# Optimization experiments

Hardware: AMD Instinct MI355X
Metric: run time of the kernel (lower is better)

## Reference

```python
import jax, jax.numpy as jnp
import numpy as np
import math

K_DIM = 1024
HEADS = 16

def setup_inputs() -> dict:
    key = jax.random.key(0)
    ks = jax.random.split(key, 6)
    b, N, k = 4, 2048, K_DIM
    sc = 1.0 / math.sqrt(k)
    return {
        "x": jax.random.normal(ks[0], (b, N, k), dtype=jnp.float32),
        "Wk": jax.random.normal(ks[1], (k, k), dtype=jnp.float32) * sc,
        "Wq": jax.random.normal(ks[2], (k, k), dtype=jnp.float32) * sc,
        "Wv": jax.random.normal(ks[3], (k, k), dtype=jnp.float32) * sc,
        "Wu": jax.random.normal(ks[4], (k, k), dtype=jnp.float32) * sc,
        "bu": jax.random.normal(ks[5], (k,), dtype=jnp.float32) * 0.01,
    }

def reference(x, Wk, Wq, Wv, Wu, bu):
    b, N, k = x.shape
    h = HEADS
    s = k // h
    # torch Linear: y = x @ W^T
    Q = (x @ Wq.T).reshape(b, N, h, s).transpose(0, 2, 1, 3)  # [b,h,N,s]
    Kh = (x @ Wk.T).reshape(b, N, h, s).transpose(0, 2, 1, 3)
    V = (x @ Wv.T).reshape(b, N, h, s).transpose(0, 2, 1, 3)
    scores = jnp.einsum('bhid,bhjd->bhij', Q, Kh) / math.sqrt(s)  # [b,h,N,N]
    attn = jax.nn.softmax(scores, axis=-1)
    out = jnp.einsum('bhij,bhjd->bhid', attn, V)  # [b,h,N,s]
    out = out.transpose(0, 2, 1, 3).reshape(b, N, k)
    return out @ Wu.T + bu
```

## Files before the change

kernel.cpp:

```cpp
#include <hip/hip_runtime.h>

typedef __bf16 bf16;
typedef __bf16 bf16x4 __attribute__((ext_vector_type(4)));
typedef __bf16 bf16x8 __attribute__((ext_vector_type(8)));
typedef float  f32x4  __attribute__((ext_vector_type(4)));

#define MFMA16(a, b, c) __builtin_amdgcn_mfma_f32_16x16x32_bf16((a), (b), (c), 0, 0, 0)

__device__ __forceinline__ void async_copy16(const void* g, void* l) {
  __builtin_amdgcn_global_load_lds(
      (const __attribute__((address_space(1))) unsigned int*)g,
      (__attribute__((address_space(3))) unsigned int*)l, 16, 0, 0);
}

struct CvtArgs {
  const float* src[5];
  bf16* dst[5];
  int blk_start[6];
};
__global__ void k_cvt_all(CvtArgs a) {
  int b = blockIdx.x;
  int seg = 0;
#pragma unroll
  for (int s = 1; s < 5; ++s) seg += (b >= a.blk_start[s]);
  int i = (b - a.blk_start[seg]) * 2048 + threadIdx.x * 8;
  float4 v0 = *(const float4*)(a.src[seg] + i);
  float4 v1 = *(const float4*)(a.src[seg] + i + 4);
  float sc = (seg == 1) ? 0.18033688f : 1.0f;
  bf16x8 o = { (bf16)(v0.x * sc), (bf16)(v0.y * sc), (bf16)(v0.z * sc), (bf16)(v0.w * sc),
               (bf16)(v1.x * sc), (bf16)(v1.y * sc), (bf16)(v1.z * sc), (bf16)(v1.w * sc) };
  *(bf16x8*)(a.dst[seg] + i) = o;
}

template <int OUTF32, int PERMB = 0>
__device__ __forceinline__ void gemm128_body(
    const bf16* __restrict__ A, const bf16* __restrict__ B, void* __restrict__ Cp,
    const float* __restrict__ bias, int m0, int n0, int N, int K) {
  __shared__ alignas(16) bf16 As[2][128 * 32];
  __shared__ alignas(16) bf16 Bs[2][128 * 32];
  const int tid = threadIdx.x;
  const int lane = tid & 63;
  const int w = tid >> 6;
  const int quad = lane >> 4;
  const int l16 = lane & 15;
  const int wr = (w >> 1) * 64;
  const int wc = (w & 1) * 64;

  const int srow = tid >> 2;
  const int skk = (tid & 3) * 8;
  const int srowB =
      PERMB ? ((srow & 0x23) | ((srow & 0x04) << 2) | ((srow & 0x18) >> 1)) : srow;
  const bf16* Ag = A + (long)(m0 + srow) * K + skk;
  const bf16* Bg = B + (long)(n0 + srowB) * K + skk;
  const long half = 64L * K;
  bf16* AsW0 = As[0] + w * 512;
  bf16* BsW0 = Bs[0] + w * 512;
  bf16* AsW1 = As[1] + w * 512;
  bf16* BsW1 = Bs[1] + w * 512;

  f32x4 acc[4][4];
#pragma unroll
  for (int i = 0; i < 4; ++i)
#pragma unroll
    for (int j = 0; j < 4; ++j) acc[i][j] = (f32x4){0.f, 0.f, 0.f, 0.f};

  for (int k0 = 0; k0 < K; k0 += 64) {
    async_copy16(Ag + k0, AsW0);
    async_copy16(Ag + half + k0, AsW0 + 2048);
    async_copy16(Bg + k0, BsW0);
    async_copy16(Bg + half + k0, BsW0 + 2048);
    async_copy16(Ag + k0 + 32, AsW1);
    async_copy16(Ag + half + k0 + 32, AsW1 + 2048);
    async_copy16(Bg + k0 + 32, BsW1);
    async_copy16(Bg + half + k0 + 32, BsW1 + 2048);
    __syncthreads();
#pragma unroll
    for (int p = 0; p < 2; ++p) {
      const bf16* AsP = As[p];
      const bf16* BsP = Bs[p];
      bf16x8 af[4], bfr[4];
#pragma unroll
      for (int i = 0; i < 4; ++i)
        af[i] = *(const bf16x8*)&AsP[(wr + i * 16 + l16) * 32 + quad * 8];
#pragma unroll
      for (int j = 0; j < 4; ++j)
        bfr[j] = *(const bf16x8*)&BsP[(wc + j * 16 + l16) * 32 + quad * 8];
#pragma unroll
      for (int i = 0; i < 4; ++i)
#pragma unroll
        for (int j = 0; j < 4; ++j) acc[i][j] = MFMA16(af[i], bfr[j], acc[i][j]);
    }
    __syncthreads();
  }

#pragma unroll
  for (int i = 0; i < 4; ++i)
#pragma unroll
    for (int j = 0; j < 4; ++j)
#pragma unroll
      for (int r = 0; r < 4; ++r) {
        long row = m0 + wr + i * 16 + quad * 4 + r;
        int col = n0 + wc + j * 16 + l16;
        if (OUTF32)
          ((float*)Cp)[row * N + col] = acc[i][j][r] + bias[col];
        else
          ((bf16*)Cp)[row * N + col] = (bf16)acc[i][j][r];
      }
}

__global__ __launch_bounds__(256, 4) void k_gemm_qkv(
    const bf16* __restrict__ xb, const bf16* __restrict__ Wqk, bf16* __restrict__ QKb,
    const bf16* __restrict__ Wvb, bf16* __restrict__ VtG) {
  int bid = blockIdx.x;
  if (bid < 1024) {
    gemm128_body<0, 0>(xb, Wqk, QKb, nullptr,
                       (bid & 63) * 128, (bid >> 6) * 128, 2048, 1024);
  } else {
    int id = bid - 1024;
    gemm128_body<0, 1>(Wvb, xb, VtG, nullptr,
                       (id >> 6) * 128, (id & 63) * 128, 8192, 1024);
  }
}

__global__ __launch_bounds__(256, 4) void k_gemm_out(
    const bf16* __restrict__ Ab, const bf16* __restrict__ Wub, float* __restrict__ out,
    const float* __restrict__ bu) {
  gemm128_body<1, 0>(Ab, Wub, out, bu, blockIdx.x * 128, blockIdx.y * 128, 1024, 1024);
}

__global__ __launch_bounds__(256, 2) void k_attn(
    const bf16* __restrict__ Q, const bf16* __restrict__ Kb,
    const bf16* __restrict__ Vt, bf16* __restrict__ O) {
  __shared__ alignas(16) bf16 Ks[2][64 * 64];
  __shared__ alignas(16) bf16 Vs[2][64 * 64];

  const int tid = threadIdx.x;
  const int lane = tid & 63;
  const int w = tid >> 6;
  const int quad = lane >> 4;
  const int l16 = lane & 15;
  const int hsw = l16 & 7;
  const int bh = blockIdx.x;
  const int qt = blockIdx.y;
  const int bb = bh >> 4;
  const int h = bh & 15;
  const int hoff = h * 64;
  const long rowQ0 = (long)bb * 2048 + qt * 256;
  const long kv0 = (long)bb * 2048;

  bf16x8 bq[4][2];
#pragma unroll
  for (int g = 0; g < 4; ++g)
#pragma unroll
    for (int ss = 0; ss < 2; ++ss)
      bq[g][ss] = *(const bf16x8*)(Q + (rowQ0 + w * 64 + g * 16 + l16) * 2048 +
                                   hoff + ss * 32 + quad * 8);

  f32x4 accO[4][4];
  f32x4 accS[4];
#pragma unroll
  for (int g = 0; g < 4; ++g) {
    accS[g] = (f32x4){0.f, 0.f, 0.f, 0.f};
#pragma unroll
    for (int t = 0; t < 4; ++t) accO[g][t] = (f32x4){0.f, 0.f, 0.f, 0.f};
  }

  const int rr = tid >> 3;
  const int cc8 = ((tid & 7) ^ (rr & 7)) * 8;
  const bf16* ksrc = Kb + (kv0 + rr) * 2048 + hoff + cc8;
  const bf16* vsrc = Vt + (long)(hoff + rr) * 8192 + kv0 + cc8;
  const int dstOff = w * 512;

  async_copy16(ksrc, Ks[0] + dstOff);
  async_copy16(ksrc + 32 * 2048, Ks[0] + 2048 + dstOff);
  async_copy16(vsrc, Vs[0] + dstOff);
  async_copy16(vsrc + 32 * 8192, Vs[0] + 2048 + dstOff);
  ksrc += 64 * 2048;
  vsrc += 64;

  const bf16 onev = (bf16)1.0f;
  const bf16x8 ones8 = {onev, onev, onev, onev, onev, onev, onev, onev};

  for (int kt = 0; kt < 32; ++kt) {
    __syncthreads();
    if (kt < 31) {
      bf16* kb = Ks[(kt + 1) & 1];
      bf16* vb = Vs[(kt + 1) & 1];
      async_copy16(ksrc, kb + dstOff);
      async_copy16(ksrc + 32 * 2048, kb + 2048 + dstOff);
      async_copy16(vsrc, vb + dstOff);
      async_copy16(vsrc + 32 * 8192, vb + 2048 + dstOff);
      ksrc += 64 * 2048;
      vsrc += 64;
    }
    const bf16* kbuf = Ks[kt & 1];
    const bf16* vbuf = Vs[kt & 1];

    bf16x8 ak[4][2];
#pragma unroll
    for (int mt = 0; mt < 4; ++mt) {
      const int rb = (mt * 16 + l16) * 64;
      ak[mt][0] = *(const bf16x8*)&kbuf[rb + ((quad ^ hsw) * 8)];
      ak[mt][1] = *(const bf16x8*)&kbuf[rb + (((4 + quad) ^ hsw) * 8)];
    }
    bf16x8 bv[2][4];
#pragma unroll
    for (int ss = 0; ss < 2; ++ss)
#pragma unroll
      for (int t = 0; t < 4; ++t) {
        const int rb = (t * 16 + l16) * 64;
        bv[ss][t] = *(const bf16x8*)&vbuf[rb + (((ss * 4 + quad) ^ hsw) * 8)];
      }

#pragma unroll
    for (int g = 0; g < 4; ++g) {
      f32x4 st[4];
      __builtin_amdgcn_s_setprio(1);
#pragma unroll
      for (int mt = 0; mt < 4; ++mt) {
        st[mt] = (f32x4){0.f, 0.f, 0.f, 0.f};
        st[mt] = MFMA16(ak[mt][0], bq[g][0], st[mt]);
        st[mt] = MFMA16(ak[mt][1], bq[g][1], st[mt]);
      }
      __builtin_amdgcn_s_setprio(0);
      bf16x8 apf[2];
#pragma unroll
      for (int mt = 0; mt < 4; ++mt) {
#pragma unroll
        for (int r = 0; r < 4; ++r) {
          float pv = __builtin_amdgcn_exp2f(st[mt][r]);
          apf[mt >> 1][(mt & 1) * 4 + r] = (bf16)pv;
        }
      }
      __builtin_amdgcn_s_setprio(1);
#pragma unroll
      for (int ss = 0; ss < 2; ++ss) {
#pragma unroll
        for (int t = 0; t < 4; ++t)
          accO[g][t] = MFMA16(apf[ss], bv[ss][t], accO[g][t]);
        accS[g] = MFMA16(apf[ss], ones8, accS[g]);
      }
      __builtin_amdgcn_s_setprio(0);
    }
  }

#pragma unroll
  for (int g = 0; g < 4; ++g)
#pragma unroll
    for (int r = 0; r < 4; ++r) {
      float inv = 1.f / accS[g][r];
      long row = rowQ0 + w * 64 + g * 16 + quad * 4 + r;
#pragma unroll
      for (int t = 0; t < 4; ++t)
        O[row * 1024 + hoff + t * 16 + l16] = (bf16)(accO[g][t][r] * inv);
    }
}

extern "C" void kernel_launch(void* const* d_in, const int* in_sizes, int n_in,
                              void* d_out, int out_size, void* d_ws, size_t ws_size,
                              hipStream_t stream) {
  const float* x  = (const float*)d_in[0];
  const float* Wk = (const float*)d_in[1];
  const float* Wq = (const float*)d_in[2];
  const float* Wv = (const float*)d_in[3];
  const float* Wu = (const float*)d_in[4];
  const float* bu = (const float*)d_in[5];
  float* out = (float*)d_out;

  const int XE = 4 * 2048 * 1024;
  const int WE = 1024 * 1024;

  bf16* p = (bf16*)d_ws;
  bf16* xb   = p; p += XE;
  bf16* Wqkb = p; p += 2 * WE;
  bf16* Wvb  = p; p += WE;
  bf16* Wub  = p; p += WE;
  bf16* QKb  = p; p += 2 * XE;
  bf16* VtG  = p; p += XE;
  bf16* Ab   = p; p += XE;

  CvtArgs ca;
  ca.src[0] = x;  ca.dst[0] = xb;
  ca.src[1] = Wq; ca.dst[1] = Wqkb;
  ca.src[2] = Wk; ca.dst[2] = Wqkb + WE;
  ca.src[3] = Wv; ca.dst[3] = Wvb;
  ca.src[4] = Wu; ca.dst[4] = Wub;
  ca.blk_start[0] = 0;
  ca.blk_start[1] = XE / 2048;
  ca.blk_start[2] = ca.blk_start[1] + WE / 2048;
  ca.blk_start[3] = ca.blk_start[2] + WE / 2048;
  ca.blk_start[4] = ca.blk_start[3] + WE / 2048;
  ca.blk_start[5] = ca.blk_start[4] + WE / 2048;
  k_cvt_all<<<ca.blk_start[5], 256, 0, stream>>>(ca);

  k_gemm_qkv<<<1536, 256, 0, stream>>>(xb, Wqkb, QKb, Wvb, VtG);

  k_attn<<<dim3(64, 8), 256, 0, stream>>>(QKb, QKb + 1024, VtG, Ab);

  k_gemm_out<<<dim3(64, 8), 256, 0, stream>>>(Ab, Wub, out, bu);
}
```

Measured before the change: 243.7 us.

## Fuse attention and output projection into one cooperative kernel with grid sync

```diff
diff --git a/kernel.cpp b/kernel.cpp
--- a/kernel.cpp
+++ b/kernel.cpp
@@ -1,4 +1,7 @@
 #include <hip/hip_runtime.h>
+#include <hip/hip_cooperative_groups.h>
+
+namespace cg = cooperative_groups;
 
 typedef __bf16 bf16;
 typedef __bf16 bf16x4 __attribute__((ext_vector_type(4)));
@@ -35,9 +38,8 @@
 template <int OUTF32, int PERMB = 0>
 __device__ __forceinline__ void gemm128_body(
     const bf16* __restrict__ A, const bf16* __restrict__ B, void* __restrict__ Cp,
-    const float* __restrict__ bias, int m0, int n0, int N, int K) {
-  __shared__ alignas(16) bf16 As[2][128 * 32];
-  __shared__ alignas(16) bf16 Bs[2][128 * 32];
+    const float* __restrict__ bias, int m0, int n0, int N, int K,
+    bf16* AsS, bf16* BsS) {
   const int tid = threadIdx.x;
   const int lane = tid & 63;
   const int w = tid >> 6;
@@ -53,10 +55,10 @@
   const bf16* Ag = A + (long)(m0 + srow) * K + skk;
   const bf16* Bg = B + (long)(n0 + srowB) * K + skk;
   const long half = 64L * K;
-  bf16* AsW0 = As[0] + w * 512;
-  bf16* BsW0 = Bs[0] + w * 512;
-  bf16* AsW1 = As[1] + w * 512;
-  bf16* BsW1 = Bs[1] + w * 512;
+  bf16* AsW0 = AsS + w * 512;
+  bf16* BsW0 = BsS + w * 512;
+  bf16* AsW1 = AsS + 4096 + w * 512;
+  bf16* BsW1 = BsS + 4096 + w * 512;
 
   f32x4 acc[4][4];
 #pragma unroll
@@ -76,8 +78,8 @@
     __syncthreads();
 #pragma unroll
     for (int p = 0; p < 2; ++p) {
-      const bf16* AsP = As[p];
-      const bf16* BsP = Bs[p];
+      const bf16* AsP = AsS + p * 4096;
+      const bf16* BsP = BsS + p * 4096;
       bf16x8 af[4], bfr[4];
 #pragma unroll
       for (int i = 0; i < 4; ++i)
@@ -111,29 +113,32 @@
 __global__ __launch_bounds__(256, 4) void k_gemm_qkv(
     const bf16* __restrict__ xb, const bf16* __restrict__ Wqk, bf16* __restrict__ QKb,
     const bf16* __restrict__ Wvb, bf16* __restrict__ VtG) {
+  __shared__ alignas(16) bf16 As[2 * 128 * 32];
+  __shared__ alignas(16) bf16 Bs[2 * 128 * 32];
   int bid = blockIdx.x;
   if (bid < 1024) {
     gemm128_body<0, 0>(xb, Wqk, QKb, nullptr,
-                       (bid & 63) * 128, (bid >> 6) * 128, 2048, 1024);
+                       (bid & 63) * 128, (bid >> 6) * 128, 2048, 1024, As, Bs);
   } else {
     int id = bid - 1024;
     gemm128_body<0, 1>(Wvb, xb, VtG, nullptr,
-                       (id >> 6) * 128, (id & 63) * 128, 8192, 1024);
+                       (id >> 6) * 128, (id & 63) * 128, 8192, 1024, As, Bs);
   }
 }
 
 __global__ __launch_bounds__(256, 4) void k_gemm_out(
     const bf16* __restrict__ Ab, const bf16* __restrict__ Wub, float* __restrict__ out,
     const float* __restrict__ bu) {
-  gemm128_body<1, 0>(Ab, Wub, out, bu, blockIdx.x * 128, blockIdx.y * 128, 1024, 1024);
-}
-
-__global__ __launch_bounds__(256, 2) void k_attn(
+  __shared__ alignas(16) bf16 As[2 * 128 * 32];
+  __shared__ alignas(16) bf16 Bs[2 * 128 * 32];
+  gemm128_body<1, 0>(Ab, Wub, out, bu, blockIdx.x * 128, blockIdx.y * 128, 1024, 1024,
+                     As, Bs);
+}
+
+__device__ __forceinline__ void attn_body(
     const bf16* __restrict__ Q, const bf16* __restrict__ Kb,
-    const bf16* __restrict__ Vt, bf16* __restrict__ O) {
-  __shared__ alignas(16) bf16 Ks[2][64 * 64];
-  __shared__ alignas(16) bf16 Vs[2][64 * 64];
-
+    const bf16* __restrict__ Vt, bf16* __restrict__ Ab,
+    bf16* KsB, bf16* VsB) {
   const int tid = threadIdx.x;
   const int lane = tid & 63;
   const int w = tid >> 6;
@@ -171,10 +176,10 @@
   const bf16* vsrc = Vt + (long)(hoff + rr) * 8192 + kv0 + cc8;
   const int dstOff = w * 512;
 
-  async_copy16(ksrc, Ks[0] + dstOff);
-  async_copy16(ksrc + 32 * 2048, Ks[0] + 2048 + dstOff);
-  async_copy16(vsrc, Vs[0] + dstOff);
-  async_copy16(vsrc + 32 * 8192, Vs[0] + 2048 + dstOff);
+  async_copy16(ksrc, KsB + dstOff);
+  async_copy16(ksrc + 32 * 2048, KsB + 2048 + dstOff);
+  async_copy16(vsrc, VsB + dstOff);
+  async_copy16(vsrc + 32 * 8192, VsB + 2048 + dstOff);
   ksrc += 64 * 2048;
   vsrc += 64;
 
@@ -184,8 +189,8 @@
   for (int kt = 0; kt < 32; ++kt) {
     __syncthreads();
     if (kt < 31) {
-      bf16* kb = Ks[(kt + 1) & 1];
-      bf16* vb = Vs[(kt + 1) & 1];
+      bf16* kb = KsB + ((kt + 1) & 1) * 4096;
+      bf16* vb = VsB + ((kt + 1) & 1) * 4096;
       async_copy16(ksrc, kb + dstOff);
       async_copy16(ksrc + 32 * 2048, kb + 2048 + dstOff);
       async_copy16(vsrc, vb + dstOff);
@@ -193,8 +198,8 @@
       ksrc += 64 * 2048;
       vsrc += 64;
     }
-    const bf16* kbuf = Ks[kt & 1];
-    const bf16* vbuf = Vs[kt & 1];
+    const bf16* kbuf = KsB + (kt & 1) * 4096;
+    const bf16* vbuf = VsB + (kt & 1) * 4096;
 
     bf16x8 ak[4][2];
 #pragma unroll
@@ -252,8 +257,34 @@
       long row = rowQ0 + w * 64 + g * 16 + quad * 4 + r;
 #pragma unroll
       for (int t = 0; t < 4; ++t)
-        O[row * 1024 + hoff + t * 16 + l16] = (bf16)(accO[g][t][r] * inv);
-    }
+        Ab[row * 1024 + hoff + t * 16 + l16] = (bf16)(accO[g][t][r] * inv);
+    }
+}
+
+__global__ __launch_bounds__(256, 2) void k_attn(
+    const bf16* __restrict__ Q, const bf16* __restrict__ Kb,
+    const bf16* __restrict__ Vt, bf16* __restrict__ O) {
+  __shared__ alignas(16) bf16 Ks[2 * 64 * 64];
+  __shared__ alignas(16) bf16 Vs[2 * 64 * 64];
+  attn_body(Q, Kb, Vt, O, Ks, Vs);
+}
+
+__global__ __launch_bounds__(256, 4) void k_attn_out(
+    const bf16* __restrict__ Q, const bf16* __restrict__ Kb,
+    const bf16* __restrict__ Vt, bf16* __restrict__ Ab,
+    const bf16* __restrict__ Wub, float* __restrict__ out,
+    const float* __restrict__ bu) {
+  __shared__ alignas(16) bf16 L0[2 * 64 * 64];
+  __shared__ alignas(16) bf16 L1[2 * 64 * 64];
+
+  attn_body(Q, Kb, Vt, Ab, L0, L1);
+
+  __threadfence();
+  cg::this_grid().sync();
+  __threadfence();
+
+  gemm128_body<1, 0>(Ab, Wub, out, bu, blockIdx.x * 128, blockIdx.y * 128, 1024, 1024,
+                     L0, L1);
 }
 
 extern "C" void kernel_launch(void* const* d_in, const int* in_sizes, int n_in,
@@ -295,7 +326,16 @@
 
   k_gemm_qkv<<<1536, 256, 0, stream>>>(xb, Wqkb, QKb, Wvb, VtG);
 
-  k_attn<<<dim3(64, 8), 256, 0, stream>>>(QKb, QKb + 1024, VtG, Ab);
-
-  k_gemm_out<<<dim3(64, 8), 256, 0, stream>>>(Ab, Wub, out, bu);
-}
+  const bf16* Qp = QKb;
+  const bf16* Kp = QKb + 1024;
+  const bf16* Vp = VtG;
+  void* args[] = {(void*)&Qp, (void*)&Kp, (void*)&Vp, (void*)&Ab,
+                  (void*)&Wub, (void*)&out, (void*)&bu};
+  hipError_t ce = hipLaunchCooperativeKernel((const void*)k_attn_out, dim3(64, 8),
+                                             dim3(256, 1, 1), args, 0, stream);
+  if (ce != hipSuccess) {
+    (void)hipGetLastError();
+    k_attn<<<dim3(64, 8), 256, 0, stream>>>(QKb, QKb + 1024, VtG, Ab);
+    k_gemm_out<<<dim3(64, 8), 256, 0, stream>>>(Ab, Wub, out, bu);
+  }
+}
```

Measured after the change: 751.8 us. 208% more time.
